# Performance work log

Measured on AMD Instinct MI355X. Metric: run time of the kernel, lower is better.

The kernel has to match this reference:

```python
import jax, jax.numpy as jnp
import numpy as np

DIM = 4          # number of trunk networks (x, y, z, t)
H = 256          # hidden width for trunk and branch MLPs
R = 64           # CP rank
FD = 1           # field_dim
NF = 64          # Fourier feature half-width (B has shape (1, 64))
BRANCH_DIM = 256
DEPTH = 3        # MLP depth (3 hidden layers per eqx.nn.MLP semantics)


def _lin_init(key, out_dim, in_dim):
    return jax.random.normal(key, (out_dim, in_dim), dtype=jnp.float32) / jnp.sqrt(jnp.float32(in_dim))


def setup_inputs() -> dict:
    key = jax.random.key(0)
    ks = jax.random.split(key, 40)
    inp = {}
    # coordinate arrays, one per trunk: (N_i, 1)
    inp['x1'] = jax.random.uniform(ks[0], (64, 1), dtype=jnp.float32)
    inp['x2'] = jax.random.uniform(ks[1], (64, 1), dtype=jnp.float32)
    inp['x3'] = jax.random.uniform(ks[2], (64, 1), dtype=jnp.float32)
    inp['x4'] = jax.random.uniform(ks[3], (32, 1), dtype=jnp.float32)
    # branch input: batch of power maps, (B, branch_dim)
    inp['f'] = jax.random.normal(ks[4], (8, BRANCH_DIM), dtype=jnp.float32)
    # Fourier feature matrix B ~ 2*pi*N(0,1), shape (1, 64)
    inp['B'] = 2.0 * jnp.pi * jax.random.normal(ks[5], (1, NF), dtype=jnp.float32)
    # trunk ensemble params, stacked over the DIM trunks (all share shapes)
    inp['tW0'] = jnp.stack([_lin_init(ks[6 + i], H, 2 * NF) for i in range(DIM)])
    inp['tb0'] = jnp.zeros((DIM, H), dtype=jnp.float32)
    inp['tW1'] = jnp.stack([_lin_init(ks[10 + i], H, H) for i in range(DIM)])
    inp['tb1'] = jnp.zeros((DIM, H), dtype=jnp.float32)
    inp['tW2'] = jnp.stack([_lin_init(ks[14 + i], H, H) for i in range(DIM)])
    inp['tb2'] = jnp.zeros((DIM, H), dtype=jnp.float32)
    inp['tW3'] = jnp.stack([_lin_init(ks[18 + i], R * FD, H) for i in range(DIM)])
    inp['tb3'] = jnp.zeros((DIM, R * FD), dtype=jnp.float32)
    # branch MLP params
    inp['bW0'] = _lin_init(ks[30], H, BRANCH_DIM)
    inp['bb0'] = jnp.zeros((H,), dtype=jnp.float32)
    inp['bW1'] = _lin_init(ks[31], H, H)
    inp['bb1'] = jnp.zeros((H,), dtype=jnp.float32)
    inp['bW2'] = _lin_init(ks[32], H, H)
    inp['bb2'] = jnp.zeros((H,), dtype=jnp.float32)
    inp['bW3'] = _lin_init(ks[33], R * FD, H)
    inp['bb3'] = jnp.zeros((R * FD,), dtype=jnp.float32)
    return inp


def _forward(x1, x2, x3, x4, f, B,
             tW0, tb0, tW1, tb1, tW2, tb2, tW3, tb3,
             bW0, bb0, bW1, bb1, bW2, bb2, bW3, bb3):
    xs = [x1, x2, x3, x4]
    ts = []
    for i in range(DIM):
        p = xs[i] @ B                                  # (N_i, NF)
        feat = jnp.concatenate([jnp.cos(p), jnp.sin(p)], axis=1)  # (N_i, 2*NF)
        h = jax.nn.swish(feat @ tW0[i].T + tb0[i])
        h = jax.nn.swish(h @ tW1[i].T + tb1[i])
        h = jax.nn.swish(h @ tW2[i].T + tb2[i])
        t = (h @ tW3[i].T + tb3[i]).reshape(-1, FD, R)  # (N_i, y, z)
        ts.append(t)
    h = jax.nn.swish(f @ bW0.T + bb0)
    h = jax.nn.swish(h @ bW1.T + bb1)
    h = jax.nn.swish(h @ bW2.T + bb2)
    b = (h @ bW3.T + bb3).reshape(-1, FD, R)            # (B, y, z)
    # rank-R CP outer-product reconstruction: sum over z, shared field dim y
    return jnp.einsum('iyz,jyz,kyz,lyz,byz->bijkly',
                      ts[0], ts[1], ts[2], ts[3], b, optimize='optimal')


def reference(x1, x2, x3, x4, f, B,
              tW0, tb0, tW1, tb1, tW2, tb2, tW3, tb3,
              bW0, bb0, bW1, bb1, bW2, bb2, bW3, bb3):
    return _forward(x1, x2, x3, x4, f, B,
                    tW0, tb0, tW1, tb1, tW2, tb2, tW3, tb3,
                    bW0, bb0, bW1, bb1, bW2, bb2, bW3, bb3)
```

## Files before the change

### kernel.cpp

```cpp
#include <hip/hip_runtime.h>
#include <math.h>


#define HID 256
#define NFF 64

__global__ __launch_bounds__(256) void net_eval(
    const float* __restrict__ x1, const float* __restrict__ x2,
    const float* __restrict__ x3, const float* __restrict__ x4,
    const float* __restrict__ f,  const float* __restrict__ Bm,
    const float* __restrict__ tW0, const float* __restrict__ tb0,
    const float* __restrict__ tW1, const float* __restrict__ tb1,
    const float* __restrict__ tW2, const float* __restrict__ tb2,
    const float* __restrict__ tW3, const float* __restrict__ tb3,
    const float* __restrict__ bW0, const float* __restrict__ bb0,
    const float* __restrict__ bW1, const float* __restrict__ bb1,
    const float* __restrict__ bW2, const float* __restrict__ bb2,
    const float* __restrict__ bW3, const float* __restrict__ bb3,
    float* __restrict__ ws)
{
    __shared__ float bufA[HID];
    __shared__ float bufB[HID];
    const int t = threadIdx.x;
    const int bid = blockIdx.x;

    int net, row;
    if (bid < 192)      { net = bid >> 6; row = bid & 63; }
    else if (bid < 224) { net = 3;        row = bid - 192; }
    else                { net = 4;        row = bid - 224; }

    const float *W0, *B0v, *W1, *B1v, *W2, *B2v, *W3, *B3v;
    int in0;
    if (net < 4) {
        W0 = tW0 + (size_t)net * HID * 2 * NFF; B0v = tb0 + net * HID;
        W1 = tW1 + (size_t)net * HID * HID;     B1v = tb1 + net * HID;
        W2 = tW2 + (size_t)net * HID * HID;     B2v = tb2 + net * HID;
        W3 = tW3 + (size_t)net * 64 * HID;      B3v = tb3 + net * 64;
        in0 = 2 * NFF;
        const float* xp = (net == 0) ? x1 : (net == 1) ? x2 : (net == 2) ? x3 : x4;
        float xv = xp[row];
        if (t < 128) {
            float p = xv * Bm[t & 63];
            bufA[t] = (t < 64) ? cosf(p) : sinf(p);
        }
    } else {
        W0 = bW0; B0v = bb0; W1 = bW1; B1v = bb1;
        W2 = bW2; B2v = bb2; W3 = bW3; B3v = bb3;
        in0 = 256;
        bufA[t] = f[(size_t)row * 256 + t];
    }
    __syncthreads();

    {
        float acc = B0v[t];
        const float4* wr = (const float4*)(W0 + (size_t)t * in0);
        const float4* iv = (const float4*)bufA;
        const int n4 = in0 >> 2;
        for (int k = 0; k < n4; ++k) {
            float4 w = wr[k]; float4 v = iv[k];
            acc += w.x * v.x + w.y * v.y + w.z * v.z + w.w * v.w;
        }
        bufB[t] = acc / (1.0f + expf(-acc));
    }
    __syncthreads();

    {
        float acc = B1v[t];
        const float4* wr = (const float4*)(W1 + (size_t)t * HID);
        const float4* iv = (const float4*)bufB;
        for (int k = 0; k < HID / 4; ++k) {
            float4 w = wr[k]; float4 v = iv[k];
            acc += w.x * v.x + w.y * v.y + w.z * v.z + w.w * v.w;
        }
        bufA[t] = acc / (1.0f + expf(-acc));
    }
    __syncthreads();

    {
        float acc = B2v[t];
        const float4* wr = (const float4*)(W2 + (size_t)t * HID);
        const float4* iv = (const float4*)bufA;
        for (int k = 0; k < HID / 4; ++k) {
            float4 w = wr[k]; float4 v = iv[k];
            acc += w.x * v.x + w.y * v.y + w.z * v.z + w.w * v.w;
        }
        bufB[t] = acc / (1.0f + expf(-acc));
    }
    __syncthreads();

    if (t < 64) {
        float acc = B3v[t];
        const float4* wr = (const float4*)(W3 + (size_t)t * HID);
        const float4* iv = (const float4*)bufB;
        for (int k = 0; k < HID / 4; ++k) {
            float4 w = wr[k]; float4 v = iv[k];
            acc += w.x * v.x + w.y * v.y + w.z * v.z + w.w * v.w;
        }
        int base, stride;
        if      (net == 0) { base = 0;     stride = 64; }
        else if (net == 1) { base = 4096;  stride = 64; }
        else if (net == 2) { base = 8192;  stride = 64; }
        else if (net == 3) { base = 12288; stride = 32; }
        else               { base = 14336; stride = 8;  }
        ws[base + t * stride + row] = acc;
    }
}

__global__ __launch_bounds__(256) void cp_recon(
    const float* __restrict__ ws, float* __restrict__ out)
{
    __shared__ float t2s[64 * 64];
    __shared__ float t3s[64 * 32];
    __shared__ float sS[4 * 64];

    const int t = threadIdx.x;
    const int bid = blockIdx.x;
    const int b  = bid >> 10;
    const int i  = (bid >> 4) & 63;
    const int j0 = (bid & 15) * 4;

    #pragma unroll
    for (int m = 0; m < 16; ++m) {
        int g = t + m * 256;
        t2s[g] = ws[8192 + g];
    }
    #pragma unroll
    for (int m = 0; m < 8; ++m) {
        int g = t + m * 256;
        t3s[g] = ws[12288 + g];
    }
    {
        int jj = t >> 6;
        int z  = t & 63;
        sS[t] = ws[z * 64 + i] * ws[4096 + z * 64 + j0 + jj] * ws[14336 + z * 8 + b];
    }
    __syncthreads();

    const int jj   = t >> 6;
    const int lane = t & 63;
    const int k0   = (lane >> 3) * 8;
    const int l0   = (lane & 7) * 4;
    const float* sp = &sS[jj * 64];

    float4 acc[8];
    #pragma unroll
    for (int kk = 0; kk < 8; ++kk) acc[kk] = make_float4(0.f, 0.f, 0.f, 0.f);

    #pragma unroll 4
    for (int z = 0; z < 64; ++z) {
        float sz = sp[z];
        float4 t3v = *(const float4*)&t3s[z * 32 + l0];
        float4 a0  = *(const float4*)&t2s[z * 64 + k0];
        float4 a1  = *(const float4*)&t2s[z * 64 + k0 + 4];
        float4 u;
        u.x = sz * t3v.x; u.y = sz * t3v.y; u.z = sz * t3v.z; u.w = sz * t3v.w;
        float ks0 = a0.x, ks1 = a0.y, ks2 = a0.z, ks3 = a0.w;
        float ks4 = a1.x, ks5 = a1.y, ks6 = a1.z, ks7 = a1.w;
        acc[0].x += ks0 * u.x; acc[0].y += ks0 * u.y; acc[0].z += ks0 * u.z; acc[0].w += ks0 * u.w;
        acc[1].x += ks1 * u.x; acc[1].y += ks1 * u.y; acc[1].z += ks1 * u.z; acc[1].w += ks1 * u.w;
        acc[2].x += ks2 * u.x; acc[2].y += ks2 * u.y; acc[2].z += ks2 * u.z; acc[2].w += ks2 * u.w;
        acc[3].x += ks3 * u.x; acc[3].y += ks3 * u.y; acc[3].z += ks3 * u.z; acc[3].w += ks3 * u.w;
        acc[4].x += ks4 * u.x; acc[4].y += ks4 * u.y; acc[4].z += ks4 * u.z; acc[4].w += ks4 * u.w;
        acc[5].x += ks5 * u.x; acc[5].y += ks5 * u.y; acc[5].z += ks5 * u.z; acc[5].w += ks5 * u.w;
        acc[6].x += ks6 * u.x; acc[6].y += ks6 * u.y; acc[6].z += ks6 * u.z; acc[6].w += ks6 * u.w;
        acc[7].x += ks7 * u.x; acc[7].y += ks7 * u.y; acc[7].z += ks7 * u.z; acc[7].w += ks7 * u.w;
    }

    size_t base = ((size_t)((b * 64 + i) * 64 + (j0 + jj))) * 2048;
    float* op = out + base;
    #pragma unroll
    for (int kk = 0; kk < 8; ++kk) {
        *(float4*)&op[(k0 + kk) * 32 + l0] = acc[kk];
    }
}

extern "C" void kernel_launch(void* const* d_in, const int* in_sizes, int n_in,
                              void* d_out, int out_size, void* d_ws, size_t ws_size,
                              hipStream_t stream) {
    const float* x1  = (const float*)d_in[0];
    const float* x2  = (const float*)d_in[1];
    const float* x3  = (const float*)d_in[2];
    const float* x4  = (const float*)d_in[3];
    const float* f   = (const float*)d_in[4];
    const float* Bm  = (const float*)d_in[5];
    const float* tW0 = (const float*)d_in[6];
    const float* tb0 = (const float*)d_in[7];
    const float* tW1 = (const float*)d_in[8];
    const float* tb1 = (const float*)d_in[9];
    const float* tW2 = (const float*)d_in[10];
    const float* tb2 = (const float*)d_in[11];
    const float* tW3 = (const float*)d_in[12];
    const float* tb3 = (const float*)d_in[13];
    const float* bW0 = (const float*)d_in[14];
    const float* bb0 = (const float*)d_in[15];
    const float* bW1 = (const float*)d_in[16];
    const float* bb1 = (const float*)d_in[17];
    const float* bW2 = (const float*)d_in[18];
    const float* bb2 = (const float*)d_in[19];
    const float* bW3 = (const float*)d_in[20];
    const float* bb3 = (const float*)d_in[21];

    float* ws  = (float*)d_ws;
    float* out = (float*)d_out;

    hipLaunchKernelGGL(net_eval, dim3(232), dim3(256), 0, stream,
                       x1, x2, x3, x4, f, Bm,
                       tW0, tb0, tW1, tb1, tW2, tb2, tW3, tb3,
                       bW0, bb0, bW1, bb1, bW2, bb2, bW3, bb3, ws);
    hipLaunchKernelGGL(cp_recon, dim3(8192), dim3(256), 0, stream, ws, out);
}
```

Before: 394.7 us.

## Compute four j values per thread in CP reconstruction and split MLP dot-product accumulators

```diff
diff --git a/kernel.cpp b/kernel.cpp
--- a/kernel.cpp
+++ b/kernel.cpp
@@ -52,50 +52,58 @@
     __syncthreads();
 
     {
-        float acc = B0v[t];
         const float4* wr = (const float4*)(W0 + (size_t)t * in0);
         const float4* iv = (const float4*)bufA;
         const int n4 = in0 >> 2;
+        float4 a4 = make_float4(0.f, 0.f, 0.f, 0.f);
         for (int k = 0; k < n4; ++k) {
             float4 w = wr[k]; float4 v = iv[k];
-            acc += w.x * v.x + w.y * v.y + w.z * v.z + w.w * v.w;
-        }
+            a4.x += w.x * v.x; a4.y += w.y * v.y;
+            a4.z += w.z * v.z; a4.w += w.w * v.w;
+        }
+        float acc = B0v[t] + ((a4.x + a4.y) + (a4.z + a4.w));
         bufB[t] = acc / (1.0f + expf(-acc));
     }
     __syncthreads();
 
     {
-        float acc = B1v[t];
         const float4* wr = (const float4*)(W1 + (size_t)t * HID);
         const float4* iv = (const float4*)bufB;
+        float4 a4 = make_float4(0.f, 0.f, 0.f, 0.f);
         for (int k = 0; k < HID / 4; ++k) {
             float4 w = wr[k]; float4 v = iv[k];
-            acc += w.x * v.x + w.y * v.y + w.z * v.z + w.w * v.w;
-        }
+            a4.x += w.x * v.x; a4.y += w.y * v.y;
+            a4.z += w.z * v.z; a4.w += w.w * v.w;
+        }
+        float acc = B1v[t] + ((a4.x + a4.y) + (a4.z + a4.w));
         bufA[t] = acc / (1.0f + expf(-acc));
     }
     __syncthreads();
 
     {
-        float acc = B2v[t];
         const float4* wr = (const float4*)(W2 + (size_t)t * HID);
         const float4* iv = (const float4*)bufA;
+        float4 a4 = make_float4(0.f, 0.f, 0.f, 0.f);
         for (int k = 0; k < HID / 4; ++k) {
             float4 w = wr[k]; float4 v = iv[k];
-            acc += w.x * v.x + w.y * v.y + w.z * v.z + w.w * v.w;
-        }
+            a4.x += w.x * v.x; a4.y += w.y * v.y;
+            a4.z += w.z * v.z; a4.w += w.w * v.w;
+        }
+        float acc = B2v[t] + ((a4.x + a4.y) + (a4.z + a4.w));
         bufB[t] = acc / (1.0f + expf(-acc));
     }
     __syncthreads();
 
     if (t < 64) {
-        float acc = B3v[t];
         const float4* wr = (const float4*)(W3 + (size_t)t * HID);
         const float4* iv = (const float4*)bufB;
+        float4 a4 = make_float4(0.f, 0.f, 0.f, 0.f);
         for (int k = 0; k < HID / 4; ++k) {
             float4 w = wr[k]; float4 v = iv[k];
-            acc += w.x * v.x + w.y * v.y + w.z * v.z + w.w * v.w;
-        }
+            a4.x += w.x * v.x; a4.y += w.y * v.y;
+            a4.z += w.z * v.z; a4.w += w.w * v.w;
+        }
+        float acc = B3v[t] + ((a4.x + a4.y) + (a4.z + a4.w));
         int base, stride;
         if      (net == 0) { base = 0;     stride = 64; }
         else if (net == 1) { base = 4096;  stride = 64; }
@@ -111,13 +119,13 @@
 {
     __shared__ float t2s[64 * 64];
     __shared__ float t3s[64 * 32];
-    __shared__ float sS[4 * 64];
+    __shared__ float sS[64 * 16];
 
     const int t = threadIdx.x;
     const int bid = blockIdx.x;
-    const int b  = bid >> 10;
-    const int i  = (bid >> 4) & 63;
-    const int j0 = (bid & 15) * 4;
+    const int b  = bid >> 8;
+    const int i  = (bid >> 2) & 63;
+    const int j0 = (bid & 3) * 16;
 
     #pragma unroll
     for (int m = 0; m < 16; ++m) {
@@ -130,9 +138,14 @@
         t3s[g] = ws[12288 + g];
     }
     {
-        int jj = t >> 6;
-        int z  = t & 63;
-        sS[t] = ws[z * 64 + i] * ws[4096 + z * 64 + j0 + jj] * ws[14336 + z * 8 + b];
+        const int jq = t & 15;
+        const int zb = t >> 4;
+        #pragma unroll
+        for (int q = 0; q < 4; ++q) {
+            int z = zb + q * 16;
+            sS[z * 16 + jq] =
+                ws[z * 64 + i] * ws[4096 + z * 64 + j0 + jq] * ws[14336 + z * 8 + b];
+        }
     }
     __syncthreads();
 
@@ -140,37 +153,47 @@
     const int lane = t & 63;
     const int k0   = (lane >> 3) * 8;
     const int l0   = (lane & 7) * 4;
-    const float* sp = &sS[jj * 64];
-
-    float4 acc[8];
-    #pragma unroll
-    for (int kk = 0; kk < 8; ++kk) acc[kk] = make_float4(0.f, 0.f, 0.f, 0.f);
-
-    #pragma unroll 4
+
+    float4 acc[4][8];
+    #pragma unroll
+    for (int jl = 0; jl < 4; ++jl)
+        #pragma unroll
+        for (int kk = 0; kk < 8; ++kk)
+            acc[jl][kk] = make_float4(0.f, 0.f, 0.f, 0.f);
+
     for (int z = 0; z < 64; ++z) {
-        float sz = sp[z];
-        float4 t3v = *(const float4*)&t3s[z * 32 + l0];
         float4 a0  = *(const float4*)&t2s[z * 64 + k0];
         float4 a1  = *(const float4*)&t2s[z * 64 + k0 + 4];
-        float4 u;
-        u.x = sz * t3v.x; u.y = sz * t3v.y; u.z = sz * t3v.z; u.w = sz * t3v.w;
-        float ks0 = a0.x, ks1 = a0.y, ks2 = a0.z, ks3 = a0.w;
-        float ks4 = a1.x, ks5 = a1.y, ks6 = a1.z, ks7 = a1.w;
-        acc[0].x += ks0 * u.x; acc[0].y += ks0 * u.y; acc[0].z += ks0 * u.z; acc[0].w += ks0 * u.w;
-        acc[1].x += ks1 * u.x; acc[1].y += ks1 * u.y; acc[1].z += ks1 * u.z; acc[1].w += ks1 * u.w;
-        acc[2].x += ks2 * u.x; acc[2].y += ks2 * u.y; acc[2].z += ks2 * u.z; acc[2].w += ks2 * u.w;
-        acc[3].x += ks3 * u.x; acc[3].y += ks3 * u.y; acc[3].z += ks3 * u.z; acc[3].w += ks3 * u.w;
-        acc[4].x += ks4 * u.x; acc[4].y += ks4 * u.y; acc[4].z += ks4 * u.z; acc[4].w += ks4 * u.w;
-        acc[5].x += ks5 * u.x; acc[5].y += ks5 * u.y; acc[5].z += ks5 * u.z; acc[5].w += ks5 * u.w;
-        acc[6].x += ks6 * u.x; acc[6].y += ks6 * u.y; acc[6].z += ks6 * u.z; acc[6].w += ks6 * u.w;
-        acc[7].x += ks7 * u.x; acc[7].y += ks7 * u.y; acc[7].z += ks7 * u.z; acc[7].w += ks7 * u.w;
-    }
-
-    size_t base = ((size_t)((b * 64 + i) * 64 + (j0 + jj))) * 2048;
-    float* op = out + base;
-    #pragma unroll
-    for (int kk = 0; kk < 8; ++kk) {
-        *(float4*)&op[(k0 + kk) * 32 + l0] = acc[kk];
+        float4 t3v = *(const float4*)&t3s[z * 32 + l0];
+        float4 s4  = *(const float4*)&sS[z * 16 + jj * 4];
+        const float ks0 = a0.x, ks1 = a0.y, ks2 = a0.z, ks3 = a0.w;
+        const float ks4 = a1.x, ks5 = a1.y, ks6 = a1.z, ks7 = a1.w;
+        #pragma unroll
+        for (int jl = 0; jl < 4; ++jl) {
+            const float sz = (jl == 0) ? s4.x : (jl == 1) ? s4.y
+                           : (jl == 2) ? s4.z : s4.w;
+            float4 u;
+            u.x = sz * t3v.x; u.y = sz * t3v.y; u.z = sz * t3v.z; u.w = sz * t3v.w;
+            acc[jl][0].x += ks0 * u.x; acc[jl][0].y += ks0 * u.y; acc[jl][0].z += ks0 * u.z; acc[jl][0].w += ks0 * u.w;
+            acc[jl][1].x += ks1 * u.x; acc[jl][1].y += ks1 * u.y; acc[jl][1].z += ks1 * u.z; acc[jl][1].w += ks1 * u.w;
+            acc[jl][2].x += ks2 * u.x; acc[jl][2].y += ks2 * u.y; acc[jl][2].z += ks2 * u.z; acc[jl][2].w += ks2 * u.w;
+            acc[jl][3].x += ks3 * u.x; acc[jl][3].y += ks3 * u.y; acc[jl][3].z += ks3 * u.z; acc[jl][3].w += ks3 * u.w;
+            acc[jl][4].x += ks4 * u.x; acc[jl][4].y += ks4 * u.y; acc[jl][4].z += ks4 * u.z; acc[jl][4].w += ks4 * u.w;
+            acc[jl][5].x += ks5 * u.x; acc[jl][5].y += ks5 * u.y; acc[jl][5].z += ks5 * u.z; acc[jl][5].w += ks5 * u.w;
+            acc[jl][6].x += ks6 * u.x; acc[jl][6].y += ks6 * u.y; acc[jl][6].z += ks6 * u.z; acc[jl][6].w += ks6 * u.w;
+            acc[jl][7].x += ks7 * u.x; acc[jl][7].y += ks7 * u.y; acc[jl][7].z += ks7 * u.z; acc[jl][7].w += ks7 * u.w;
+        }
+    }
+
+    #pragma unroll
+    for (int jl = 0; jl < 4; ++jl) {
+        const int j = j0 + jj * 4 + jl;
+        size_t base = ((size_t)((b * 64 + i) * 64 + j)) * 2048;
+        float* op = out + base;
+        #pragma unroll
+        for (int kk = 0; kk < 8; ++kk) {
+            *(float4*)&op[(k0 + kk) * 32 + l0] = acc[jl][kk];
+        }
     }
 }
 
@@ -207,5 +230,5 @@
                        x1, x2, x3, x4, f, Bm,
                        tW0, tb0, tW1, tb1, tW2, tb2, tW3, tb3,
                        bW0, bb0, bW1, bb1, bW2, bb2, bW3, bb3, ws);
-    hipLaunchKernelGGL(cp_recon, dim3(8192), dim3(256), 0, stream, ws, out);
+    hipLaunchKernelGGL(cp_recon, dim3(2048), dim3(256), 0, stream, ws, out);
 }
```

After: 396.2 us. No clear change (+0.4%).
